# Kernel tuning notes

Measured on AMD Instinct MI355X. Metric: run time of the kernel, lower is better.

Reference implementation:

```python
import jax, jax.numpy as jnp
import numpy as np

B, C, H, W, D = 16, 512, 14, 14, 8000  # batch, channels(=input_dim1=input_dim2), spatial, output_dim


def _sketch_matrix(seed_h, seed_s, input_dim, output_dim):
    # Reproduce the module's count-sketch matrix generation (np.random.seed based).
    np.random.seed(seed_h)
    rand_h = np.random.randint(output_dim, size=input_dim)
    np.random.seed(seed_s)
    rand_s = (2 * np.random.randint(2, size=input_dim) - 1).astype(np.float32)
    M = np.zeros((input_dim, output_dim), dtype=np.float32)
    M[np.arange(input_dim), rand_h] = rand_s  # one-hot-per-row with sign
    return jnp.asarray(M)


def setup_inputs() -> dict:
    key = jax.random.key(0)
    x = jax.random.normal(key, (B, C, H, W), dtype=jnp.float32)
    S1 = _sketch_matrix(1, 3, C, D)
    S2 = _sketch_matrix(5, 7, C, D)
    return {"x": x, "S1": S1, "S2": S2}


def reference(x, S1, S2):
    b, c, h, w = x.shape
    # NCHW -> (B*H*W, C)
    flat = jnp.transpose(x, (0, 2, 3, 1)).reshape(-1, c)
    sketch1 = flat @ S1  # [BHW, D]
    sketch2 = flat @ S2  # [BHW, D]
    # circular convolution of the two count-sketches via FFT
    f1 = jnp.fft.fft(sketch1, axis=-1)
    f2 = jnp.fft.fft(sketch2, axis=-1)
    cbp_flat = jnp.fft.ifft(f1 * f2, axis=-1).real.astype(x.dtype)
    cbp = cbp_flat.reshape(b, h, w, -1)
    # sum_pool=True: reduce over spatial dims -> [B, D]
    return cbp.sum(axis=(1, 2))
```

## Files before the change

kernel.cpp:

```cpp
#include <hip/hip_runtime.h>

#define B_DIM 16
#define C_DIM 512
#define HW_DIM 196
#define D_DIM 8000

#define KT 28
#define BT 128
#define PAD 4

__global__ __launch_bounds__(256) void extract_both(
    const float* __restrict__ S1, const float* __restrict__ S2,
    int* __restrict__ h, float* __restrict__ s) {
    const int row   = blockIdx.x & (C_DIM - 1);
    const int which = blockIdx.x >> 9;
    const float* S  = which ? S2 : S1;
    const float4* rowp = (const float4*)(S + (size_t)row * D_DIM);
    int*   hp = h + which * C_DIM;
    float* sp = s + which * C_DIM;
    for (int j4 = threadIdx.x; j4 < D_DIM / 4; j4 += 256) {
        float4 v = rowp[j4];
        if (v.x != 0.0f) { hp[row] = 4 * j4 + 0; sp[row] = v.x; }
        if (v.y != 0.0f) { hp[row] = 4 * j4 + 1; sp[row] = v.y; }
        if (v.z != 0.0f) { hp[row] = 4 * j4 + 2; sp[row] = v.z; }
        if (v.w != 0.0f) { hp[row] = 4 * j4 + 3; sp[row] = v.w; }
    }
}

__global__ __launch_bounds__(256) void gram_hist(
    const float* __restrict__ x,
    const int* __restrict__ h1, const float* __restrict__ s1,
    const int* __restrict__ h2, const float* __restrict__ s2,
    float* __restrict__ part) {
    const int b  = blockIdx.z;
    const int i0 = blockIdx.y * BT;
    const int j0 = blockIdx.x * BT;
    const float* A = x + (size_t)b * C_DIM * HW_DIM;

    __shared__ float hist[D_DIM];
    __shared__ float At[KT][BT + PAD];
    __shared__ float Bt[KT][BT + PAD];

    const int tid = threadIdx.x;
    const int tx  = tid & 15;
    const int ty  = tid >> 4;

    for (int d = tid; d < D_DIM; d += 256) hist[d] = 0.0f;

    float acc[8][8] = {};

    for (int k0 = 0; k0 < HW_DIM; k0 += KT) {
        #pragma unroll
        for (int l = 0; l < 14; ++l) {
            int idx = l * 256 + tid;
            int r   = idx / KT;
            int kk  = idx - r * KT;
            int k   = k0 + kk;
            At[kk][r] = A[(size_t)(i0 + r) * HW_DIM + k];
            Bt[kk][r] = A[(size_t)(j0 + r) * HW_DIM + k];
        }
        __syncthreads();

        #pragma unroll
        for (int kk = 0; kk < KT; ++kk) {
            float4 a0 = *(const float4*)&At[kk][ty * 8];
            float4 a1 = *(const float4*)&At[kk][ty * 8 + 4];
            float4 b0 = *(const float4*)&Bt[kk][tx * 8];
            float4 b1 = *(const float4*)&Bt[kk][tx * 8 + 4];
            float a[8] = {a0.x, a0.y, a0.z, a0.w, a1.x, a1.y, a1.z, a1.w};
            float bb[8] = {b0.x, b0.y, b0.z, b0.w, b1.x, b1.y, b1.z, b1.w};
            #pragma unroll
            for (int u = 0; u < 8; ++u)
                #pragma unroll
                for (int v = 0; v < 8; ++v)
                    acc[u][v] += a[u] * bb[v];
        }
        __syncthreads();
    }

    int hr[8]; float sr[8]; int hc[8]; float sc[8];
    #pragma unroll
    for (int u = 0; u < 8; ++u) {
        hr[u] = h1[i0 + ty * 8 + u];
        sr[u] = s1[i0 + ty * 8 + u];
    }
    #pragma unroll
    for (int v = 0; v < 8; ++v) {
        hc[v] = h2[j0 + tx * 8 + v];
        sc[v] = s2[j0 + tx * 8 + v];
    }
    #pragma unroll
    for (int u = 0; u < 8; ++u)
        #pragma unroll
        for (int v = 0; v < 8; ++v) {
            int bin = hr[u] + hc[v];
            if (bin >= D_DIM) bin -= D_DIM;
            atomicAdd(&hist[bin], sr[u] * sc[v] * acc[u][v]);
        }
    __syncthreads();

    float* pb = part + (size_t)((b * 4 + blockIdx.y) * 4 + blockIdx.x) * D_DIM;
    for (int d = tid; d < D_DIM; d += 256) pb[d] = hist[d];
}

__global__ __launch_bounds__(256) void reduce_part(
    const float* __restrict__ part, float* __restrict__ out) {
    int idx = blockIdx.x * 256 + threadIdx.x;
    if (idx >= B_DIM * D_DIM) return;
    int b = idx / D_DIM;
    int d = idx - b * D_DIM;
    const float* p = part + (size_t)b * 16 * D_DIM + d;
    float v = 0.0f;
    #pragma unroll
    for (int t = 0; t < 16; ++t) v += p[(size_t)t * D_DIM];
    out[idx] = v;
}

extern "C" void kernel_launch(void* const* d_in, const int* in_sizes, int n_in,
                              void* d_out, int out_size, void* d_ws, size_t ws_size,
                              hipStream_t stream) {
    const float* x  = (const float*)d_in[0];
    const float* S1 = (const float*)d_in[1];
    const float* S2 = (const float*)d_in[2];
    float* out = (float*)d_out;

    int*   h    = (int*)d_ws;
    float* s    = (float*)(h + 2 * C_DIM);
    float* part = s + 2 * C_DIM;

    extract_both<<<2 * C_DIM, 256, 0, stream>>>(S1, S2, h, s);

    dim3 grid(C_DIM / BT, C_DIM / BT, B_DIM);
    gram_hist<<<grid, 256, 0, stream>>>(x, h, s, h + C_DIM, s + C_DIM, part);

    reduce_part<<<(B_DIM * D_DIM + 255) / 256, 256, 0, stream>>>(part, out);
}
```

Baseline: 133.3 us.

## Halve gram tile width, raise occupancy, and reduce partial histograms via global atomics

The per-block Gram tile shrinks from 128x128 to 128x64, which doubles the grid to 512 blocks and gives each thread an 8x4 accumulator, with launch_bounds asking for two blocks per CU. The separate partial-buffer write and reduce kernel are replaced by a memset of the output followed by global atomicAdd of each block's non-zero shared-histogram bins. The aim is better CU occupancy and fewer launches and partial-buffer traffic. The cost is twice the redundant x reads per batch, more blocks each zeroing and scanning an 8000-entry LDS histogram, and contended global atomics with non-deterministic summation order.

After: 138.2 us. 1.04x slower.

```diff
diff --git a/kernel.cpp b/kernel.cpp
--- a/kernel.cpp
+++ b/kernel.cpp
@@ -6,7 +6,8 @@
 #define D_DIM 8000
 
 #define KT 28
-#define BT 128
+#define IT 128
+#define JT 64
 #define PAD 4
 
 __global__ __launch_bounds__(256) void extract_both(
@@ -27,19 +28,19 @@
     }
 }
 
-__global__ __launch_bounds__(256) void gram_hist(
+__global__ __launch_bounds__(256, 2) void gram_hist(
     const float* __restrict__ x,
     const int* __restrict__ h1, const float* __restrict__ s1,
     const int* __restrict__ h2, const float* __restrict__ s2,
-    float* __restrict__ part) {
+    float* __restrict__ out) {
     const int b  = blockIdx.z;
-    const int i0 = blockIdx.y * BT;
-    const int j0 = blockIdx.x * BT;
+    const int i0 = blockIdx.y * IT;
+    const int j0 = blockIdx.x * JT;
     const float* A = x + (size_t)b * C_DIM * HW_DIM;
 
     __shared__ float hist[D_DIM];
-    __shared__ float At[KT][BT + PAD];
-    __shared__ float Bt[KT][BT + PAD];
+    __shared__ float At[KT][IT + PAD];
+    __shared__ float Bt[KT][JT + PAD];
 
     const int tid = threadIdx.x;
     const int tx  = tid & 15;
@@ -47,7 +48,7 @@
 
     for (int d = tid; d < D_DIM; d += 256) hist[d] = 0.0f;
 
-    float acc[8][8] = {};
+    float acc[8][4] = {};
 
     for (int k0 = 0; k0 < HW_DIM; k0 += KT) {
         #pragma unroll
@@ -55,9 +56,14 @@
             int idx = l * 256 + tid;
             int r   = idx / KT;
             int kk  = idx - r * KT;
-            int k   = k0 + kk;
-            At[kk][r] = A[(size_t)(i0 + r) * HW_DIM + k];
-            Bt[kk][r] = A[(size_t)(j0 + r) * HW_DIM + k];
+            At[kk][r] = A[(size_t)(i0 + r) * HW_DIM + k0 + kk];
+        }
+        #pragma unroll
+        for (int l = 0; l < 7; ++l) {
+            int idx = l * 256 + tid;
+            int r   = idx / KT;
+            int kk  = idx - r * KT;
+            Bt[kk][r] = A[(size_t)(j0 + r) * HW_DIM + k0 + kk];
         }
         __syncthreads();
 
@@ -65,55 +71,44 @@
         for (int kk = 0; kk < KT; ++kk) {
             float4 a0 = *(const float4*)&At[kk][ty * 8];
             float4 a1 = *(const float4*)&At[kk][ty * 8 + 4];
-            float4 b0 = *(const float4*)&Bt[kk][tx * 8];
-            float4 b1 = *(const float4*)&Bt[kk][tx * 8 + 4];
-            float a[8] = {a0.x, a0.y, a0.z, a0.w, a1.x, a1.y, a1.z, a1.w};
-            float bb[8] = {b0.x, b0.y, b0.z, b0.w, b1.x, b1.y, b1.z, b1.w};
+            float4 b0 = *(const float4*)&Bt[kk][tx * 4];
+            float a[8]  = {a0.x, a0.y, a0.z, a0.w, a1.x, a1.y, a1.z, a1.w};
+            float bb[4] = {b0.x, b0.y, b0.z, b0.w};
             #pragma unroll
             for (int u = 0; u < 8; ++u)
                 #pragma unroll
-                for (int v = 0; v < 8; ++v)
+                for (int v = 0; v < 4; ++v)
                     acc[u][v] += a[u] * bb[v];
         }
         __syncthreads();
     }
 
-    int hr[8]; float sr[8]; int hc[8]; float sc[8];
+    int hr[8]; float sr[8]; int hc[4]; float sc[4];
     #pragma unroll
     for (int u = 0; u < 8; ++u) {
         hr[u] = h1[i0 + ty * 8 + u];
         sr[u] = s1[i0 + ty * 8 + u];
     }
     #pragma unroll
-    for (int v = 0; v < 8; ++v) {
-        hc[v] = h2[j0 + tx * 8 + v];
-        sc[v] = s2[j0 + tx * 8 + v];
+    for (int v = 0; v < 4; ++v) {
+        hc[v] = h2[j0 + tx * 4 + v];
+        sc[v] = s2[j0 + tx * 4 + v];
     }
     #pragma unroll
     for (int u = 0; u < 8; ++u)
         #pragma unroll
-        for (int v = 0; v < 8; ++v) {
+        for (int v = 0; v < 4; ++v) {
             int bin = hr[u] + hc[v];
             if (bin >= D_DIM) bin -= D_DIM;
             atomicAdd(&hist[bin], sr[u] * sc[v] * acc[u][v]);
         }
     __syncthreads();
 
-    float* pb = part + (size_t)((b * 4 + blockIdx.y) * 4 + blockIdx.x) * D_DIM;
-    for (int d = tid; d < D_DIM; d += 256) pb[d] = hist[d];
-}
-
-__global__ __launch_bounds__(256) void reduce_part(
-    const float* __restrict__ part, float* __restrict__ out) {
-    int idx = blockIdx.x * 256 + threadIdx.x;
-    if (idx >= B_DIM * D_DIM) return;
-    int b = idx / D_DIM;
-    int d = idx - b * D_DIM;
-    const float* p = part + (size_t)b * 16 * D_DIM + d;
-    float v = 0.0f;
-    #pragma unroll
-    for (int t = 0; t < 16; ++t) v += p[(size_t)t * D_DIM];
-    out[idx] = v;
+    float* outb = out + (size_t)b * D_DIM;
+    for (int d = tid; d < D_DIM; d += 256) {
+        float v = hist[d];
+        if (v != 0.0f) atomicAdd(outb + d, v);
+    }
 }
 
 extern "C" void kernel_launch(void* const* d_in, const int* in_sizes, int n_in,
@@ -124,14 +119,13 @@
     const float* S2 = (const float*)d_in[2];
     float* out = (float*)d_out;
 
-    int*   h    = (int*)d_ws;
-    float* s    = (float*)(h + 2 * C_DIM);
-    float* part = s + 2 * C_DIM;
+    int*   h = (int*)d_ws;
+    float* s = (float*)(h + 2 * C_DIM);
+
+    hipMemsetAsync(d_out, 0, (size_t)out_size * sizeof(float), stream);
 
     extract_both<<<2 * C_DIM, 256, 0, stream>>>(S1, S2, h, s);
 
-    dim3 grid(C_DIM / BT, C_DIM / BT, B_DIM);
-    gram_hist<<<grid, 256, 0, stream>>>(x, h, s, h + C_DIM, s + C_DIM, part);
-
-    reduce_part<<<(B_DIM * D_DIM + 255) / 256, 256, 0, stream>>>(part, out);
+    dim3 grid(C_DIM / JT, C_DIM / IT, B_DIM);
+    gram_hist<<<grid, 256, 0, stream>>>(x, h, s, h + C_DIM, s + C_DIM, out);
 }
```
